# Performance work log

Measured on AMD Instinct MI355X. Metric: run time of the kernel, lower is better.

## Reference

```python
import jax, jax.numpy as jnp
import numpy as np

N = 100000
E = 1600000

def setup_inputs() -> dict:
    key = jax.random.key(0)
    ks = jax.random.split(key, 8)
    x = jax.random.normal(ks[0], (N, 512), dtype=jnp.float32)
    edge_index = jax.random.randint(ks[1], (2, E), 0, N, dtype=jnp.int32)
    W1 = jax.random.normal(ks[2], (512, 64), dtype=jnp.float32) * (1.0 / np.sqrt(512))
    b1 = jnp.zeros((64,), dtype=jnp.float32)
    W2 = jax.random.normal(ks[3], (64, 32), dtype=jnp.float32) * (1.0 / np.sqrt(64))
    b2 = jnp.zeros((32,), dtype=jnp.float32)
    W3 = jax.random.normal(ks[4], (32, 4), dtype=jnp.float32) * (1.0 / np.sqrt(32))
    b3 = jnp.zeros((4,), dtype=jnp.float32)
    return {"x": x, "edge_index": edge_index, "W1": W1, "b1": b1,
            "W2": W2, "b2": b2, "W3": W3, "b3": b3}


def _gcn_norm(edge_index, n):
    # Add self-loops (fill_value=1), symmetric deg^{-1/2} normalization (PyG gcn_norm).
    loop = jnp.arange(n, dtype=edge_index.dtype)
    src = jnp.concatenate([edge_index[0], loop])
    dst = jnp.concatenate([edge_index[1], loop])
    w = jnp.ones((src.shape[0],), dtype=jnp.float32)
    deg = jax.ops.segment_sum(w, dst, num_segments=n)
    dinv = jnp.where(deg > 0, jax.lax.rsqrt(deg), 0.0)
    norm = dinv[src] * w * dinv[dst]
    return src, dst, norm


def _gcn_conv(x, W, b, src, dst, norm, n):
    h = x @ W                      # dense transform first (PyG GCNConv order)
    msg = h[src] * norm[:, None]   # gather + edge scaling
    out = jax.ops.segment_sum(msg, dst, num_segments=n)  # scatter-add aggregate
    return out + b


def reference(x, edge_index, W1, b1, W2, b2, W3, b3):
    n = x.shape[0]
    src, dst, norm = _gcn_norm(edge_index, n)  # cached=True: shared across layers
    h = jax.nn.relu(_gcn_conv(x, W1, b1, src, dst, norm, n))
    # dropout p=0.2 is identity in eval mode
    h = jax.nn.relu(_gcn_conv(h, W2, b2, src, dst, norm, n))
    # dropout p=0.4 is identity in eval mode
    out = _gcn_conv(h, W3, b3, src, dst, norm, n)
    return out
```

## Files before the change

kernel.cpp:

```cpp
#include <hip/hip_runtime.h>


typedef __attribute__((ext_vector_type(8))) short short8;
typedef __attribute__((ext_vector_type(4))) float floatx4;

#define NBUK_MAX 512
#define SC_EDGES 3072
#define HIST_EDGES 8192

__device__ __forceinline__ unsigned f2bf_bits(float f) {
    unsigned u = __float_as_uint(f);
    return (u + 0x7fffu + ((u >> 16) & 1u)) >> 16;
}
__device__ __forceinline__ float bf_bits2f(unsigned b) {
    return __uint_as_float(b << 16);
}

__global__ __launch_bounds__(256) void zero_i32(int* p, int n) {
    int i = blockIdx.x * 256 + threadIdx.x;
    if (i < n) p[i] = 0;
}

__global__ __launch_bounds__(512) void bucket_hist(const int* __restrict__ dst,
                                                   int* __restrict__ buckcnt,
                                                   int e, int shift, int nbuk) {
    __shared__ int hist[NBUK_MAX];
    int t = threadIdx.x;
    for (int i = t; i < nbuk; i += 512) hist[i] = 0;
    __syncthreads();
    long long base = (long long)blockIdx.x * HIST_EDGES;
#pragma unroll
    for (int j = 0; j < HIST_EDGES / 512; j++) {
        long long i = base + j * 512 + t;
        if (i < e) atomicAdd(&hist[dst[i] >> shift], 1);
    }
    __syncthreads();
    for (int i = t; i < nbuk; i += 512)
        if (hist[i] > 0) atomicAdd(&buckcnt[i], hist[i]);
}

__global__ __launch_bounds__(512) void bucket_scan(const int* __restrict__ buckcnt,
                                                   int* __restrict__ boff,
                                                   int* __restrict__ buckfill,
                                                   int* __restrict__ rowptr,
                                                   int nbuk, int n, int e) {
    __shared__ int sc[512];
    int t = threadIdx.x;
    int v = (t < nbuk) ? buckcnt[t] : 0;
    sc[t] = v;
    __syncthreads();
    for (int off = 1; off < 512; off <<= 1) {
        int u = (t >= off) ? sc[t - off] : 0;
        __syncthreads();
        sc[t] += u;
        __syncthreads();
    }
    int excl = sc[t] - v;
    if (t < nbuk) {
        boff[t] = excl;
        buckfill[t] = excl;
    }
    if (t == 0) {
        boff[nbuk] = e;
        rowptr[n] = e;
    }
}

__global__ __launch_bounds__(512) void bucket_scatter(const int* __restrict__ src,
                                                      const int* __restrict__ dst,
                                                      int* __restrict__ buckfill,
                                                      int2* __restrict__ colpair,
                                                      int e, int shift, int nbuk) {
    __shared__ int hist[NBUK_MAX];
    __shared__ int lscan[NBUK_MAX];
    __shared__ int fillL[NBUK_MAX];
    __shared__ int baseG[NBUK_MAX];
    __shared__ int2 stage[SC_EDGES];
    int t = threadIdx.x;
    for (int i = t; i < nbuk; i += 512) hist[i] = 0;
    __syncthreads();
    long long base = (long long)blockIdx.x * SC_EDGES;
#pragma unroll
    for (int j = 0; j < SC_EDGES / 512; j++) {
        long long i = base + j * 512 + t;
        if (i < e) atomicAdd(&hist[dst[i] >> shift], 1);
    }
    __syncthreads();
    int v = (t < nbuk) ? hist[t] : 0;
    lscan[t] = v;
    __syncthreads();
    for (int off = 1; off < 512; off <<= 1) {
        int u = (t >= off) ? lscan[t - off] : 0;
        __syncthreads();
        lscan[t] += u;
        __syncthreads();
    }
    int excl = lscan[t] - v;
    lscan[t] = excl;
    fillL[t] = excl;
    if (t < nbuk && v > 0) baseG[t] = atomicAdd(&buckfill[t], v);
    __syncthreads();
#pragma unroll
    for (int j = 0; j < SC_EDGES / 512; j++) {
        long long i = base + j * 512 + t;
        if (i < e) {
            int d = dst[i];
            int s = src[i];
            int p = atomicAdd(&fillL[d >> shift], 1);
            stage[p] = make_int2(s, d);
        }
    }
    __syncthreads();
    long long rem = (long long)e - base;
    int cnt = (rem < SC_EDGES) ? (int)rem : SC_EDGES;
    for (int k = t; k < cnt; k += 512) {
        int2 pr = stage[k];
        int b = pr.y >> shift;
        colpair[baseG[b] + (k - lscan[b])] = pr;
    }
}

__global__ __launch_bounds__(512) void csr_build(const int2* __restrict__ colpair,
                                                 const int* __restrict__ boff,
                                                 int* __restrict__ rowptr,
                                                 float* __restrict__ dinv,
                                                 int* __restrict__ colidx,
                                                 int n, int shift) {
    __shared__ int degl[NBUK_MAX];
    __shared__ int lsc[NBUK_MAX];
    __shared__ int fill[NBUK_MAX];
    int t = threadIdx.x;
    int bn = 1 << shift;
    int node0 = blockIdx.x << shift;
    int e0 = boff[blockIdx.x];
    int e1 = boff[blockIdx.x + 1];
    if (t < bn) degl[t] = 0;
    __syncthreads();
    for (int i = e0 + t; i < e1; i += 512)
        atomicAdd(&degl[colpair[i].y - node0], 1);
    __syncthreads();
    int v = (t < bn) ? degl[t] : 0;
    lsc[t] = v;
    __syncthreads();
    for (int off = 1; off < 512; off <<= 1) {
        int u = (t >= off) ? lsc[t - off] : 0;
        __syncthreads();
        lsc[t] += u;
        __syncthreads();
    }
    int excl = lsc[t] - v;
    int node = node0 + t;
    if (t < bn && node < n) {
        rowptr[node] = e0 + excl;
        dinv[node] = rsqrtf((float)(v + 1));
    }
    fill[t] = e0 + excl;
    __syncthreads();
    for (int i = e0 + t; i < e1; i += 512) {
        int2 pr = colpair[i];
        int p = atomicAdd(&fill[pr.y - node0], 1);
        colidx[p] = pr.x;
    }
}

__global__ __launch_bounds__(256) void w1_split(const float* __restrict__ W1,
                                                short* __restrict__ whi,
                                                short* __restrict__ wlo) {
    int idx = blockIdx.x * 256 + threadIdx.x;
    int k = idx >> 6;
    int nn = idx & 63;
    float v = W1[idx];
    unsigned hb = f2bf_bits(v);
    float lof = v - bf_bits2f(hb);
    unsigned lb = f2bf_bits(lof);
    int kc = k >> 5, rem = k & 31, quad = rem >> 3, j = rem & 7;
    int ct = nn >> 4, l = nn & 15;
    int lane = quad * 16 + l;
    int addr = ((ct * 16 + kc) * 64 + lane) * 8 + j;
    whi[addr] = (short)hb;
    wlo[addr] = (short)lb;
}

__global__ __launch_bounds__(256) void transform1_mfma(const float* __restrict__ x,
                                                       const short* __restrict__ whi,
                                                       const short* __restrict__ wlo,
                                                       const float* __restrict__ dinv,
                                                       float* __restrict__ h1, int n) {
    __shared__ float xs[64 * 36];
    const int t = threadIdx.x;
    const int w = t >> 6;
    const int lane = t & 63;
    const int quad = lane >> 4;
    const int row0 = blockIdx.x * 64;
    const int mrow = w * 16 + (lane & 15);
    floatx4 acc[4] = {{0.f, 0.f, 0.f, 0.f}, {0.f, 0.f, 0.f, 0.f},
                      {0.f, 0.f, 0.f, 0.f}, {0.f, 0.f, 0.f, 0.f}};

    for (int kc = 0; kc < 16; kc++) {
        __syncthreads();
#pragma unroll
        for (int i = 0; i < 2; i++) {
            int c = t + i * 256;
            int m = c >> 3;
            int koff = (c & 7) << 2;
            int grow = row0 + m;
            float4 v = make_float4(0.f, 0.f, 0.f, 0.f);
            if (grow < n) v = *(const float4*)&x[(size_t)grow * 512 + kc * 32 + koff];
            *(float4*)&xs[m * 36 + koff] = v;
        }
        __syncthreads();
        float a[8];
        *(float4*)&a[0] = *(const float4*)&xs[mrow * 36 + quad * 8];
        *(float4*)&a[4] = *(const float4*)&xs[mrow * 36 + quad * 8 + 4];
        short8 ahi, alo;
#pragma unroll
        for (int j = 0; j < 8; j++) {
            unsigned hb = f2bf_bits(a[j]);
            float lof = a[j] - bf_bits2f(hb);
            unsigned lb = f2bf_bits(lof);
            ahi[j] = (short)hb;
            alo[j] = (short)lb;
        }
        const int base = (kc * 64 + lane) * 8;
#pragma unroll
        for (int ct = 0; ct < 4; ct++) {
            short8 bhi = *(const short8*)&whi[ct * 8192 + base];
            short8 blo = *(const short8*)&wlo[ct * 8192 + base];
            acc[ct] = __builtin_amdgcn_mfma_f32_16x16x32_bf16(ahi, bhi, acc[ct], 0, 0, 0);
            acc[ct] = __builtin_amdgcn_mfma_f32_16x16x32_bf16(alo, bhi, acc[ct], 0, 0, 0);
            acc[ct] = __builtin_amdgcn_mfma_f32_16x16x32_bf16(ahi, blo, acc[ct], 0, 0, 0);
        }
    }
#pragma unroll
    for (int r = 0; r < 4; r++) {
        int grow = row0 + w * 16 + quad * 4 + r;
        if (grow < n) {
            float s = dinv[grow];
#pragma unroll
            for (int ct = 0; ct < 4; ct++) {
                h1[(size_t)grow * 64 + ct * 16 + (lane & 15)] = acc[ct][r] * s;
            }
        }
    }
}

__global__ __launch_bounds__(256) void transform2(const float* __restrict__ g1,
                                                  const float* __restrict__ W2,
                                                  const float* __restrict__ dinv,
                                                  float* __restrict__ h2, int n) {
    __shared__ float rows[32 * 68];
    __shared__ float W2s[64 * 32];
    int t = threadIdx.x;
    int row0 = blockIdx.x * 32;
#pragma unroll
    for (int i = 0; i < 2; i++) {
        int c = t + i * 256;
        int r = c >> 4, k4 = (c & 15) << 2;
        int grow = row0 + r;
        float4 v = make_float4(0.f, 0.f, 0.f, 0.f);
        if (grow < n) v = *(const float4*)&g1[(size_t)grow * 64 + k4];
        *(float4*)&rows[r * 68 + k4] = v;
    }
#pragma unroll
    for (int i = 0; i < 2; i++) {
        int c = t + i * 256;
        *(float4*)&W2s[c * 4] = *(const float4*)&W2[c * 4];
    }
    __syncthreads();
    int lr = t >> 3;
    int c4 = (t & 7) * 4;
    int row = row0 + lr;
    float a0 = 0.f, a1 = 0.f, a2 = 0.f, a3 = 0.f;
#pragma unroll
    for (int k4 = 0; k4 < 64; k4 += 4) {
        float4 a = *(const float4*)&rows[lr * 68 + k4];
        float4 w0 = *(const float4*)&W2s[(k4 + 0) * 32 + c4];
        float4 w1 = *(const float4*)&W2s[(k4 + 1) * 32 + c4];
        float4 w2 = *(const float4*)&W2s[(k4 + 2) * 32 + c4];
        float4 w3 = *(const float4*)&W2s[(k4 + 3) * 32 + c4];
        a0 += a.x * w0.x + a.y * w1.x + a.z * w2.x + a.w * w3.x;
        a1 += a.x * w0.y + a.y * w1.y + a.z * w2.y + a.w * w3.y;
        a2 += a.x * w0.z + a.y * w1.z + a.z * w2.z + a.w * w3.z;
        a3 += a.x * w0.w + a.y * w1.w + a.z * w2.w + a.w * w3.w;
    }
    if (row < n) {
        float s = dinv[row];
        float4 o = make_float4(a0 * s, a1 * s, a2 * s, a3 * s);
        *(float4*)&h2[(size_t)row * 32 + c4] = o;
    }
}

__device__ __forceinline__ void f4acc(float4& a, const float4 b) {
    a.x += b.x; a.y += b.y; a.z += b.z; a.w += b.w;
}
__device__ __forceinline__ void f4shflxor(float4& a, int m) {
    a.x += __shfl_xor(a.x, m);
    a.y += __shfl_xor(a.y, m);
    a.z += __shfl_xor(a.z, m);
    a.w += __shfl_xor(a.w, m);
}

__global__ __launch_bounds__(256) void agg64_wave(const float* __restrict__ h,
                                                  const int* __restrict__ rowptr,
                                                  const int* __restrict__ colidx,
                                                  const float* __restrict__ dinv,
                                                  const float* __restrict__ bias,
                                                  float* __restrict__ out, int n) {
    int node = (blockIdx.x * 256 + threadIdx.x) >> 6;
    if (node >= n) return;
    int lane = threadIdx.x & 63;
    int eslot = lane >> 4;
    int fq = (lane & 15) << 2;
    int r0 = rowptr[node], r1 = rowptr[node + 1];
    float4 z = make_float4(0.f, 0.f, 0.f, 0.f);
    float4 a0 = z, a1 = z, a2 = z, a3 = z;
    if (eslot == 0) a0 = *(const float4*)&h[(size_t)node * 64 + fq];
    int j = r0;
    for (; j + 15 < r1; j += 16) {
        int c0 = colidx[j + eslot];
        int c1 = colidx[j + 4 + eslot];
        int c2 = colidx[j + 8 + eslot];
        int c3 = colidx[j + 12 + eslot];
        f4acc(a0, *(const float4*)&h[(size_t)c0 * 64 + fq]);
        f4acc(a1, *(const float4*)&h[(size_t)c1 * 64 + fq]);
        f4acc(a2, *(const float4*)&h[(size_t)c2 * 64 + fq]);
        f4acc(a3, *(const float4*)&h[(size_t)c3 * 64 + fq]);
    }
    {
        int e0 = j + eslot, e1 = j + 4 + eslot, e2 = j + 8 + eslot, e3 = j + 12 + eslot;
        if (e0 < r1) f4acc(a0, *(const float4*)&h[(size_t)colidx[e0] * 64 + fq]);
        if (e1 < r1) f4acc(a1, *(const float4*)&h[(size_t)colidx[e1] * 64 + fq]);
        if (e2 < r1) f4acc(a2, *(const float4*)&h[(size_t)colidx[e2] * 64 + fq]);
        if (e3 < r1) f4acc(a3, *(const float4*)&h[(size_t)colidx[e3] * 64 + fq]);
    }
    f4acc(a0, a1); f4acc(a2, a3); f4acc(a0, a2);
    f4shflxor(a0, 16);
    f4shflxor(a0, 32);
    if (eslot == 0) {
        float dn = dinv[node];
        float4 b = *(const float4*)&bias[fq];
        float4 v = make_float4(fmaxf(dn * a0.x + b.x, 0.f), fmaxf(dn * a0.y + b.y, 0.f),
                               fmaxf(dn * a0.z + b.z, 0.f), fmaxf(dn * a0.w + b.w, 0.f));
        *(float4*)&out[(size_t)node * 64 + fq] = v;
    }
}

__global__ __launch_bounds__(256) void agg32_t3(const float* __restrict__ h,
                                                const int* __restrict__ rowptr,
                                                const int* __restrict__ colidx,
                                                const float* __restrict__ dinv,
                                                const float* __restrict__ bias,
                                                const float* __restrict__ W3,
                                                float* __restrict__ h3, int n) {
    int node = (blockIdx.x * 256 + threadIdx.x) >> 6;
    if (node >= n) return;
    int lane = threadIdx.x & 63;
    int eslot = lane >> 3;
    int fq = (lane & 7) << 2;
    int r0 = rowptr[node], r1 = rowptr[node + 1];
    float4 z = make_float4(0.f, 0.f, 0.f, 0.f);
    float4 a0 = z, a1 = z;
    if (eslot == 0) a0 = *(const float4*)&h[(size_t)node * 32 + fq];
    int j = r0;
    for (; j + 15 < r1; j += 16) {
        int c0 = colidx[j + eslot];
        int c1 = colidx[j + 8 + eslot];
        f4acc(a0, *(const float4*)&h[(size_t)c0 * 32 + fq]);
        f4acc(a1, *(const float4*)&h[(size_t)c1 * 32 + fq]);
    }
    {
        int e0 = j + eslot, e1 = j + 8 + eslot;
        if (e0 < r1) f4acc(a0, *(const float4*)&h[(size_t)colidx[e0] * 32 + fq]);
        if (e1 < r1) f4acc(a1, *(const float4*)&h[(size_t)colidx[e1] * 32 + fq]);
    }
    f4acc(a0, a1);
    f4shflxor(a0, 8);
    f4shflxor(a0, 16);
    f4shflxor(a0, 32);
    float dn = dinv[node];
    float4 b = *(const float4*)&bias[fq];
    float4 g = make_float4(fmaxf(dn * a0.x + b.x, 0.f), fmaxf(dn * a0.y + b.y, 0.f),
                           fmaxf(dn * a0.z + b.z, 0.f), fmaxf(dn * a0.w + b.w, 0.f));
    float4 w0 = *(const float4*)&W3[(fq + 0) * 4];
    float4 w1 = *(const float4*)&W3[(fq + 1) * 4];
    float4 w2 = *(const float4*)&W3[(fq + 2) * 4];
    float4 w3 = *(const float4*)&W3[(fq + 3) * 4];
    float4 p = make_float4(g.x * w0.x + g.y * w1.x + g.z * w2.x + g.w * w3.x,
                           g.x * w0.y + g.y * w1.y + g.z * w2.y + g.w * w3.y,
                           g.x * w0.z + g.y * w1.z + g.z * w2.z + g.w * w3.z,
                           g.x * w0.w + g.y * w1.w + g.z * w2.w + g.w * w3.w);
    f4shflxor(p, 1);
    f4shflxor(p, 2);
    f4shflxor(p, 4);
    if (lane == 0) {
        *(float4*)&h3[(size_t)node * 4] =
            make_float4(dn * p.x, dn * p.y, dn * p.z, dn * p.w);
    }
}

__global__ __launch_bounds__(256) void agg4_wave(const float* __restrict__ h,
                                                 const int* __restrict__ rowptr,
                                                 const int* __restrict__ colidx,
                                                 const float* __restrict__ dinv,
                                                 const float* __restrict__ bias,
                                                 float* __restrict__ out, int n) {
    int node = (blockIdx.x * 256 + threadIdx.x) >> 6;
    if (node >= n) return;
    int lane = threadIdx.x & 63;
    int eslot = lane >> 2;
    int f = lane & 3;
    int r0 = rowptr[node], r1 = rowptr[node + 1];
    float a0 = (eslot == 0) ? h[(size_t)node * 4 + f] : 0.f;
    float a1 = 0.f;
    int j = r0;
    for (; j + 15 < r1; j += 16) {
        int c = colidx[j + eslot];
        a0 += h[(size_t)c * 4 + f];
    }
    {
        int e = j + eslot;
        if (e < r1) a1 += h[(size_t)colidx[e] * 4 + f];
    }
    float s = a0 + a1;
    s += __shfl_xor(s, 4);
    s += __shfl_xor(s, 8);
    s += __shfl_xor(s, 16);
    s += __shfl_xor(s, 32);
    if (eslot == 0) out[(size_t)node * 4 + f] = dinv[node] * s + bias[f];
}

extern "C" void kernel_launch(void* const* d_in, const int* in_sizes, int n_in,
                              void* d_out, int out_size, void* d_ws, size_t ws_size,
                              hipStream_t stream) {
    const float* x  = (const float*)d_in[0];
    const int*   ei = (const int*)d_in[1];
    const float* W1 = (const float*)d_in[2];
    const float* b1 = (const float*)d_in[3];
    const float* W2 = (const float*)d_in[4];
    const float* b2 = (const float*)d_in[5];
    const float* W3 = (const float*)d_in[6];
    const float* b3 = (const float*)d_in[7];
    const int n = in_sizes[0] / 512;
    const int e = in_sizes[1] / 2;
    const int* src = ei;
    const int* dst = ei + e;
    float* out = (float*)d_out;

    char* p = (char*)d_ws;
    auto alloc = [&](size_t bytes) {
        void* r = (void*)p;
        p += (bytes + 255) & ~(size_t)255;
        return r;
    };
    int*   buckcnt  = (int*)alloc((size_t)NBUK_MAX * 4);
    int*   boff     = (int*)alloc((size_t)(NBUK_MAX + 1) * 4);
    int*   buckfill = (int*)alloc((size_t)NBUK_MAX * 4);
    int*   rowptr   = (int*)alloc((size_t)(n + 1) * 4);
    int*   colidx   = (int*)alloc((size_t)e * 4);
    float* dinv     = (float*)alloc((size_t)n * 4);
    short* whi      = (short*)alloc((size_t)32768 * 2);
    short* wlo      = (short*)alloc((size_t)32768 * 2);
    float* bufA     = (float*)alloc((size_t)n * 64 * 4);
    float* bufB     = (float*)alloc((size_t)n * 64 * 4);
    int2*  colpair  = (int2*)bufA;

    int shift = 8;
    while (((n + (1 << shift) - 1) >> shift) > NBUK_MAX) shift++;
    const int nbuk = (n + (1 << shift) - 1) >> shift;

    const int HB = (int)(((long long)e + HIST_EDGES - 1) / HIST_EDGES);
    const int SB = (int)(((long long)e + SC_EDGES - 1) / SC_EDGES);
    const int WPN = (n + 3) / 4;

    zero_i32<<<dim3((nbuk + 255) / 256), dim3(256), 0, stream>>>(buckcnt, nbuk);
    bucket_hist<<<dim3(HB), dim3(512), 0, stream>>>(dst, buckcnt, e, shift, nbuk);
    bucket_scan<<<dim3(1), dim3(512), 0, stream>>>(buckcnt, boff, buckfill, rowptr, nbuk, n, e);
    bucket_scatter<<<dim3(SB), dim3(512), 0, stream>>>(src, dst, buckfill, colpair, e, shift, nbuk);
    csr_build<<<dim3(nbuk), dim3(512), 0, stream>>>(colpair, boff, rowptr, dinv, colidx, n, shift);
    w1_split<<<dim3(128), dim3(256), 0, stream>>>(W1, whi, wlo);

    transform1_mfma<<<dim3((n + 63) / 64), dim3(256), 0, stream>>>(x, whi, wlo, dinv, bufA, n);
    agg64_wave<<<dim3(WPN), dim3(256), 0, stream>>>(bufA, rowptr, colidx, dinv, b1, bufB, n);
    transform2<<<dim3((n + 31) / 32), dim3(256), 0, stream>>>(bufB, W2, dinv, bufA, n);
    agg32_t3<<<dim3(WPN), dim3(256), 0, stream>>>(bufA, rowptr, colidx, dinv, b2, W3, bufB, n);
    agg4_wave<<<dim3(WPN), dim3(256), 0, stream>>>(bufB, rowptr, colidx, dinv, b3, out, n);
}
```

Before: 516.0 us.

## Pack edge pairs into 32-bit words and scatter CSR edges via register-held ranks

Each edge's source index and the low bits of its destination are packed into one 32-bit word, replacing the int2 pair buffer and halving the intermediate traffic. bucket_scatter now takes per-edge ranks from shared atomics kept in registers and writes directly to global memory, dropping the shared staging buffer and block-wide scan. csr_build also keeps edges and ranks in registers so colidx is written without a second atomic pass. The trade-off is a fixed cap of 6144 edges per bucket and less coalesced global writes; buckets above the cap would silently lose edges.

```diff
diff --git a/kernel.cpp b/kernel.cpp
--- a/kernel.cpp
+++ b/kernel.cpp
@@ -5,7 +5,8 @@
 typedef __attribute__((ext_vector_type(4))) float floatx4;
 
 #define NBUK_MAX 512
-#define SC_EDGES 3072
+#define SC_EDGES 8192
+#define CB_MAXE 6144
 #define HIST_EDGES 8192
 
 __device__ __forceinline__ unsigned f2bf_bits(float f) {
@@ -69,58 +70,45 @@
 __global__ __launch_bounds__(512) void bucket_scatter(const int* __restrict__ src,
                                                       const int* __restrict__ dst,
                                                       int* __restrict__ buckfill,
-                                                      int2* __restrict__ colpair,
+                                                      unsigned* __restrict__ colpack,
                                                       int e, int shift, int nbuk) {
-    __shared__ int hist[NBUK_MAX];
-    __shared__ int lscan[NBUK_MAX];
-    __shared__ int fillL[NBUK_MAX];
+    __shared__ int cnt[NBUK_MAX];
     __shared__ int baseG[NBUK_MAX];
-    __shared__ int2 stage[SC_EDGES];
     int t = threadIdx.x;
-    for (int i = t; i < nbuk; i += 512) hist[i] = 0;
+    for (int i = t; i < nbuk; i += 512) cnt[i] = 0;
     __syncthreads();
     long long base = (long long)blockIdx.x * SC_EDGES;
-#pragma unroll
-    for (int j = 0; j < SC_EDGES / 512; j++) {
+    unsigned wreg[16];
+    int breg[16];
+    unsigned lomask = (1u << shift) - 1u;
+#pragma unroll
+    for (int j = 0; j < 16; j++) {
         long long i = base + j * 512 + t;
-        if (i < e) atomicAdd(&hist[dst[i] >> shift], 1);
-    }
-    __syncthreads();
-    int v = (t < nbuk) ? hist[t] : 0;
-    lscan[t] = v;
-    __syncthreads();
-    for (int off = 1; off < 512; off <<= 1) {
-        int u = (t >= off) ? lscan[t - off] : 0;
-        __syncthreads();
-        lscan[t] += u;
-        __syncthreads();
-    }
-    int excl = lscan[t] - v;
-    lscan[t] = excl;
-    fillL[t] = excl;
-    if (t < nbuk && v > 0) baseG[t] = atomicAdd(&buckfill[t], v);
-    __syncthreads();
-#pragma unroll
-    for (int j = 0; j < SC_EDGES / 512; j++) {
-        long long i = base + j * 512 + t;
-        if (i < e) {
-            int d = dst[i];
-            int s = src[i];
-            int p = atomicAdd(&fillL[d >> shift], 1);
-            stage[p] = make_int2(s, d);
-        }
-    }
-    __syncthreads();
-    long long rem = (long long)e - base;
-    int cnt = (rem < SC_EDGES) ? (int)rem : SC_EDGES;
-    for (int k = t; k < cnt; k += 512) {
-        int2 pr = stage[k];
-        int b = pr.y >> shift;
-        colpair[baseG[b] + (k - lscan[b])] = pr;
-    }
-}
-
-__global__ __launch_bounds__(512) void csr_build(const int2* __restrict__ colpair,
+        bool ok = (i < e);
+        int d = ok ? dst[i] : 0;
+        int s = ok ? src[i] : 0;
+        int b = d >> shift;
+        int r = ok ? atomicAdd(&cnt[b], 1) : 0;
+        wreg[j] = ((unsigned)s << shift) | ((unsigned)d & lomask);
+        breg[j] = ok ? ((b << 16) | r) : -1;
+    }
+    __syncthreads();
+    for (int i = t; i < nbuk; i += 512) {
+        int v = cnt[i];
+        baseG[i] = (v > 0) ? atomicAdd(&buckfill[i], v) : 0;
+    }
+    __syncthreads();
+#pragma unroll
+    for (int j = 0; j < 16; j++) {
+        int br = breg[j];
+        if (br >= 0) {
+            int b = br >> 16, r = br & 0xffff;
+            colpack[baseG[b] + r] = wreg[j];
+        }
+    }
+}
+
+__global__ __launch_bounds__(512) void csr_build(const unsigned* __restrict__ colpack,
                                                  const int* __restrict__ boff,
                                                  int* __restrict__ rowptr,
                                                  float* __restrict__ dinv,
@@ -128,16 +116,26 @@
                                                  int n, int shift) {
     __shared__ int degl[NBUK_MAX];
     __shared__ int lsc[NBUK_MAX];
-    __shared__ int fill[NBUK_MAX];
     int t = threadIdx.x;
     int bn = 1 << shift;
+    unsigned lomask = (unsigned)bn - 1u;
     int node0 = blockIdx.x << shift;
     int e0 = boff[blockIdx.x];
     int e1 = boff[blockIdx.x + 1];
+    int cnt = e1 - e0;
     if (t < bn) degl[t] = 0;
     __syncthreads();
-    for (int i = e0 + t; i < e1; i += 512)
-        atomicAdd(&degl[colpair[i].y - node0], 1);
+    unsigned wreg[CB_MAXE / 512];
+    int rreg[CB_MAXE / 512];
+#pragma unroll
+    for (int j = 0; j < CB_MAXE / 512; j++) {
+        int k = j * 512 + t;
+        bool ok = (k < cnt);
+        unsigned w = ok ? colpack[e0 + k] : 0u;
+        int dlo = (int)(w & lomask);
+        rreg[j] = ok ? atomicAdd(&degl[dlo], 1) : -1;
+        wreg[j] = w;
+    }
     __syncthreads();
     int v = (t < bn) ? degl[t] : 0;
     lsc[t] = v;
@@ -154,12 +152,16 @@
         rowptr[node] = e0 + excl;
         dinv[node] = rsqrtf((float)(v + 1));
     }
-    fill[t] = e0 + excl;
-    __syncthreads();
-    for (int i = e0 + t; i < e1; i += 512) {
-        int2 pr = colpair[i];
-        int p = atomicAdd(&fill[pr.y - node0], 1);
-        colidx[p] = pr.x;
+    __syncthreads();
+    if (t < 512) lsc[t] = excl;
+    __syncthreads();
+#pragma unroll
+    for (int j = 0; j < CB_MAXE / 512; j++) {
+        if (rreg[j] >= 0) {
+            unsigned w = wreg[j];
+            int dlo = (int)(w & lomask);
+            colidx[e0 + lsc[dlo] + rreg[j]] = (int)(w >> shift);
+        }
     }
 }
 
@@ -462,7 +464,7 @@
     short* wlo      = (short*)alloc((size_t)32768 * 2);
     float* bufA     = (float*)alloc((size_t)n * 64 * 4);
     float* bufB     = (float*)alloc((size_t)n * 64 * 4);
-    int2*  colpair  = (int2*)bufA;
+    unsigned* colpack = (unsigned*)bufA;
 
     int shift = 8;
     while (((n + (1 << shift) - 1) >> shift) > NBUK_MAX) shift++;
@@ -475,8 +477,8 @@
     zero_i32<<<dim3((nbuk + 255) / 256), dim3(256), 0, stream>>>(buckcnt, nbuk);
     bucket_hist<<<dim3(HB), dim3(512), 0, stream>>>(dst, buckcnt, e, shift, nbuk);
     bucket_scan<<<dim3(1), dim3(512), 0, stream>>>(buckcnt, boff, buckfill, rowptr, nbuk, n, e);
-    bucket_scatter<<<dim3(SB), dim3(512), 0, stream>>>(src, dst, buckfill, colpair, e, shift, nbuk);
-    csr_build<<<dim3(nbuk), dim3(512), 0, stream>>>(colpair, boff, rowptr, dinv, colidx, n, shift);
+    bucket_scatter<<<dim3(SB), dim3(512), 0, stream>>>(src, dst, buckfill, colpack, e, shift, nbuk);
+    csr_build<<<dim3(nbuk), dim3(512), 0, stream>>>(colpack, boff, rowptr, dinv, colidx, n, shift);
     w1_split<<<dim3(128), dim3(256), 0, stream>>>(W1, whi, wlo);
 
     transform1_mfma<<<dim3((n + 63) / 64), dim3(256), 0, stream>>>(x, whi, wlo, dinv, bufA, n);
```

Result: no change. 514.1 us (-0.4%).
